# Optimization experiments

Hardware: AMD Instinct MI355X
Metric: run time of the kernel (lower is better)

## Reference

```python
import jax, jax.numpy as jnp
from jax import lax
import numpy as np

LEVEL_HW = [(100, 100), (50, 50), (25, 25), (13, 13), (7, 7)]  # P3..P7 for 800x800 input
N, C, A, K, NCONV = 2, 256, 9, 80, 4
PRIOR_PROB = 0.01


def conv3x3(x, w, b):
    # x: (N,C,H,W), w: (O,I,3,3), stride 1, pad 1
    y = lax.conv_general_dilated(x, w, (1, 1), 'SAME',
                                 dimension_numbers=('NCHW', 'OIHW', 'NCHW'))
    return y + b[None, :, None, None]


def permute_to_N_HWA_K(t, k):
    # (N, A*k, H, W) -> (N, H*W*A, k), matching the torch helper
    n, _, h, w = t.shape
    return t.reshape(n, -1, k, h, w).transpose(0, 3, 4, 1, 2).reshape(n, -1, k)


def setup_inputs() -> dict:
    key = jax.random.key(0)
    ks = iter(jax.random.split(key, 64))
    inp = {}
    for i, (h, w) in enumerate(LEVEL_HW):
        inp[f"f{i}"] = jax.random.normal(next(ks), (N, C, h, w), jnp.float32)
    for pre in ("cls", "box"):
        for i in range(NCONV):
            inp[f"{pre}_w{i}"] = 0.01 * jax.random.normal(next(ks), (C, C, 3, 3), jnp.float32)
            inp[f"{pre}_b{i}"] = jnp.zeros((C,), jnp.float32)
    bias_value = -float(np.log((1.0 - PRIOR_PROB) / PRIOR_PROB))
    inp["cls_score_w"] = 0.01 * jax.random.normal(next(ks), (A * K, C, 3, 3), jnp.float32)
    inp["cls_score_b"] = jnp.full((A * K,), bias_value, jnp.float32)
    inp["box_pred_w"] = 0.01 * jax.random.normal(next(ks), (A * 4, C, 3, 3), jnp.float32)
    inp["box_pred_b"] = jnp.zeros((A * 4,), jnp.float32)
    return inp


def reference(f0, f1, f2, f3, f4,
              cls_w0, cls_b0, cls_w1, cls_b1, cls_w2, cls_b2, cls_w3, cls_b3,
              box_w0, box_b0, box_w1, box_b1, box_w2, box_b2, box_w3, box_b3,
              cls_score_w, cls_score_b, box_pred_w, box_pred_b):
    feats = [f0, f1, f2, f3, f4]
    cls_p = [(cls_w0, cls_b0), (cls_w1, cls_b1), (cls_w2, cls_b2), (cls_w3, cls_b3)]
    box_p = [(box_w0, box_b0), (box_w1, box_b1), (box_w2, box_b2), (box_w3, box_b3)]
    logits, boxes = [], []
    for f in feats:
        x = f
        for w, b in cls_p:
            x = jax.nn.relu(conv3x3(x, w, b))
        logits.append(permute_to_N_HWA_K(conv3x3(x, cls_score_w, cls_score_b), K))
        y = f
        for w, b in box_p:
            y = jax.nn.relu(conv3x3(y, w, b))
        boxes.append(permute_to_N_HWA_K(conv3x3(y, box_pred_w, box_pred_b), 4))
    # (N, R, K) and (N, R, 4) with R = sum_l Hl*Wl*A = 120087; concat on last dim
    return jnp.concatenate([jnp.concatenate(logits, 1), jnp.concatenate(boxes, 1)], axis=2)
```

## Files before the change

kernel.cpp:

```cpp
#include <hip/hip_runtime.h>


typedef __attribute__((ext_vector_type(8))) short short8;
typedef __attribute__((ext_vector_type(4))) float floatx4;

#define LVLTOT 14143

__device__ __forceinline__ unsigned short f2bf(float f) {
  unsigned int u = __float_as_uint(f);
  unsigned int r = (u + 0x7fffu + ((u >> 16) & 1u)) >> 16;
  return (unsigned short)r;
}

__device__ __forceinline__ void gload_lds16(const void* g, void* l) {
  __builtin_amdgcn_global_load_lds(
      (const __attribute__((address_space(1))) unsigned int*)g,
      (__attribute__((address_space(3))) unsigned int*)l, 16, 0, 0);
}

__global__ __launch_bounds__(256) void xprep(
    const float* __restrict__ f, unsigned short* __restrict__ x0,
    int H, int W, int Wp, int lvloff) {
  __shared__ float ts[8][33];
  int t = threadIdx.x;
  int w0 = blockIdx.x * 32, h = blockIdx.y;
  int n = blockIdx.z >> 5, cbk = blockIdx.z & 31;
  int cl = t >> 5, wl = t & 31;
  float v = 0.f;
  if (w0 + wl < W)
    v = f[(((size_t)n * 256 + cbk * 8 + cl) * H + h) * W + w0 + wl];
  ts[cl][wl] = v;
  __syncthreads();
  int pi = t >> 3, cj = t & 7;
  if (w0 + pi < W)
    x0[((size_t)n * LVLTOT + lvloff + (size_t)(h + 1) * Wp + (w0 + pi + 1)) * 256 +
       cbk * 8 + cj] = f2bf(ts[cj][pi]);
}

struct WPArgs {
  const float* src[10];
  unsigned short* dst[10];
  int cout[10];
  int coutp[10];
};
__global__ __launch_bounds__(256) void wprep(WPArgs A) {
  int id = blockIdx.y;
  int idx = blockIdx.x * 256 + threadIdx.x;
  int coutp = A.coutp[id];
  if (idx >= coutp * 256) return;
  int co = idx >> 8, ci = idx & 255;
  const float* w = A.src[id];
  unsigned short* dst = A.dst[id];
  int cb = co >> 6, col = co & 63, chk = ci >> 5, qd = (ci >> 3) & 3, j = ci & 7;
  bool valid = co < A.cout[id];
#pragma unroll
  for (int tap = 0; tap < 9; tap++) {
    float v = valid ? w[((size_t)co * 256 + ci) * 9 + tap] : 0.f;
    dst[((((size_t)(cb * 8 + chk) * 9 + tap) * 4 + qd) * 64 + col) * 8 + j] = f2bf(v);
  }
}

__device__ __forceinline__ void decode_tile(int tile, int& l, int& h0, int& w0,
                                            int& H, int& W, int& Wp, int& loff) {
  const int Ht[5] = {100, 50, 25, 13, 7};
  const int Wpt[5] = {102, 52, 27, 15, 9};
  const int TXt[5] = {7, 4, 2, 1, 1};
  const int LOFFt[5] = {0, 10404, 13108, 13837, 14062};
  int tloc;
  if (tile < 49) { l = 0; tloc = tile; }
  else if (tile < 65) { l = 1; tloc = tile - 49; }
  else if (tile < 69) { l = 2; tloc = tile - 65; }
  else if (tile < 70) { l = 3; tloc = tile - 69; }
  else { l = 4; tloc = 0; }
  H = Ht[l]; W = H; Wp = Wpt[l]; loff = LOFFt[l];
  int ty = tloc / TXt[l], tx = tloc - ty * TXt[l];
  h0 = ty * 16; w0 = tx * 16;
}

#define CONV_MAIN_LOOP(INP, WBLOB, CB)                                          \
  for (int ch = 0; ch < 8; ch++) {                                              \
    if (ch) __syncthreads();                                                    \
    const unsigned short* wsrc = (WBLOB) + ((size_t)((CB)*8 + ch)) * 18432;     \
    _Pragma("unroll")                                                           \
    for (int i = 0; i < 9; i++)                                                 \
      gload_lds16(wsrc + i * 2048 + wv * 512 + lane * 8,                        \
                  lds_w + i * 2048 + wv * 512);                                 \
    _Pragma("unroll")                                                           \
    for (int g = 0; g < 6; g++) {                                               \
      int px = g * 64 + lane;                                                   \
      int r = px / 18, c = px - r * 18;                                         \
      int hh = h0 + r; if (hh > Hpad - 1) hh = Hpad - 1;                        \
      int ww = w0 + c; if (ww > Wp - 1) ww = Wp - 1;                            \
      gload_lds16((INP) + ((size_t)hh * Wp + ww) * 256 + ch * 32 + wv * 8,      \
                  lds_x + wv * 3072 + g * 512);                                 \
    }                                                                           \
    __syncthreads();                                                            \
    const short8* xw = (const short8*)lds_w;                                    \
    const short8* xx = (const short8*)lds_x;                                    \
    _Pragma("unroll")                                                           \
    for (int tap = 0; tap < 9; tap++) {                                         \
      const int tdy = tap / 3, tdx = tap - 3 * (tap / 3);                       \
      short8 bfr[4];                                                            \
      _Pragma("unroll")                                                         \
      for (int rr = 0; rr < 4; rr++)                                            \
        bfr[rr] = xx[q * 384 + (wv * 4 + rr + tdy) * 18 + n16 + tdx];           \
      _Pragma("unroll")                                                         \
      for (int cc = 0; cc < 4; cc++) {                                          \
        short8 afr = xw[(tap * 4 + q) * 64 + cc * 16 + n16];                    \
        _Pragma("unroll")                                                       \
        for (int rr = 0; rr < 4; rr++)                                          \
          acc[cc][rr] = __builtin_amdgcn_mfma_f32_16x16x32_bf16(                \
              afr, bfr[rr], acc[cc][rr], 0, 0, 0);                              \
      }                                                                         \
    }                                                                           \
  }

__global__ __launch_bounds__(256, 2) void conv_tower_mfma(
    const unsigned short* __restrict__ xin, unsigned short* __restrict__ xout,
    const unsigned short* __restrict__ wblob_cls,
    const unsigned short* __restrict__ wblob_box,
    const float* __restrict__ bias_cls, const float* __restrict__ bias_box,
    int in_n_stride, int in_tw_stride) {
  __shared__ __align__(16) unsigned short lds_w[18432];
  __shared__ __align__(16) unsigned short lds_x[12288];
  const int t = threadIdx.x, lane = t & 63, wv = t >> 6;
  const int q = lane >> 4, n16 = lane & 15;
  int l, h0, w0, H, W, Wp, loff;
  decode_tile(blockIdx.x, l, h0, w0, H, W, Wp, loff);
  const int Hpad = H + 2;
  const int cb = blockIdx.y;
  const int n = blockIdx.z >> 1, tw = blockIdx.z & 1;
  const unsigned short* wblob = tw ? wblob_box : wblob_cls;
  const float* bias = tw ? bias_box : bias_cls;
  const unsigned short* inp =
      xin + ((size_t)n * in_n_stride + (size_t)tw * in_tw_stride + loff) * 256;
  unsigned short* outp = xout + ((size_t)(n * 2 + tw) * LVLTOT + loff) * 256;

  floatx4 acc[4][4];
#pragma unroll
  for (int i = 0; i < 4; i++)
#pragma unroll
    for (int jj = 0; jj < 4; jj++) acc[i][jj] = (floatx4){0.f, 0.f, 0.f, 0.f};

  CONV_MAIN_LOOP(inp, wblob, cb)

#pragma unroll
  for (int cc = 0; cc < 4; cc++) {
    floatx4 bb = *(const floatx4*)(bias + cb * 64 + cc * 16 + q * 4);
#pragma unroll
    for (int rr = 0; rr < 4; rr++) {
      int h = h0 + wv * 4 + rr;
      int w_ = w0 + n16;
      if (h < H && w_ < W) {
        unsigned short pk[4];
#pragma unroll
        for (int rg = 0; rg < 4; rg++)
          pk[rg] = f2bf(fmaxf(acc[cc][rr][rg] + bb[rg], 0.f));
        size_t base =
            ((size_t)(h + 1) * Wp + (w_ + 1)) * 256 + cb * 64 + cc * 16 + q * 4;
        *(unsigned long long*)(outp + base) = *(unsigned long long*)pk;
      }
    }
  }
}

template <bool IS_CLS>
__global__ __launch_bounds__(256, 2) void conv_final_mfma(
    const unsigned short* __restrict__ xin, float* __restrict__ out,
    const unsigned short* __restrict__ wblob, const float* __restrict__ bias) {
  __shared__ __align__(16) unsigned short lds_w[18432];
  __shared__ __align__(16) unsigned short lds_x[12288];
  const int t = threadIdx.x, lane = t & 63, wv = t >> 6;
  const int q = lane >> 4, n16 = lane & 15;
  int l, h0, w0, H, W, Wp, loff;
  decode_tile(blockIdx.x, l, h0, w0, H, W, Wp, loff);
  const int Hpad = H + 2;
  const int cb = blockIdx.y;
  const int n = blockIdx.z;
  const int tw = IS_CLS ? 0 : 1;
  const int Cout = IS_CLS ? 720 : 36;
  const int RB[5] = {0, 90000, 112500, 118125, 119646};
  const unsigned short* inp = xin + ((size_t)(n * 2 + tw) * LVLTOT + loff) * 256;

  floatx4 acc[4][4];
#pragma unroll
  for (int i = 0; i < 4; i++)
#pragma unroll
    for (int jj = 0; jj < 4; jj++) acc[i][jj] = (floatx4){0.f, 0.f, 0.f, 0.f};

  CONV_MAIN_LOOP(inp, wblob, cb)

#pragma unroll
  for (int cc = 0; cc < 4; cc++) {
    int co0 = cb * 64 + cc * 16 + q * 4;
    if (co0 >= Cout) continue;
    floatx4 bb = *(const floatx4*)(bias + co0);
    int a = IS_CLS ? (co0 / 80) : (co0 >> 2);
    int col0 = IS_CLS ? (co0 - a * 80) : 80;
#pragma unroll
    for (int rr = 0; rr < 4; rr++) {
      int h = h0 + wv * 4 + rr;
      int w_ = w0 + n16;
      if (h < H && w_ < W) {
        size_t ridx = (size_t)RB[l] + ((size_t)h * W + w_) * 9 + a;
        floatx4 v;
#pragma unroll
        for (int rg = 0; rg < 4; rg++) v[rg] = acc[cc][rr][rg] + bb[rg];
        *(floatx4*)(out + ((size_t)n * 120087 + ridx) * 84 + col0) = v;
      }
    }
  }
}

extern "C" void kernel_launch(void* const* d_in, const int* in_sizes, int n_in,
                              void* d_out, int out_size, void* d_ws,
                              size_t ws_size, hipStream_t stream) {
  char* ws = (char*)d_ws;
  unsigned short* bufB = (unsigned short*)(ws);
  unsigned short* X0 = (unsigned short*)(ws + 14482432);
  unsigned short* bufA = (unsigned short*)(ws + 28964864);
  unsigned short* tb[8];
  for (int i = 0; i < 8; i++)
    tb[i] = (unsigned short*)(ws + 57929728 + (size_t)i * 1179648);
  unsigned short* fb_cls = (unsigned short*)(ws + 67366912);
  unsigned short* fb_box = (unsigned short*)(ws + 70905856);

  const float* f[5];
  for (int i = 0; i < 5; i++) f[i] = (const float*)d_in[i];
  float* out = (float*)d_out;

  hipMemsetAsync(ws, 0, 57929728, stream);

  const int Ht[5] = {100, 50, 25, 13, 7};
  const int Wpt[5] = {102, 52, 27, 15, 9};
  const int LOFFt[5] = {0, 10404, 13108, 13837, 14062};
  for (int l = 0; l < 5; l++) {
    dim3 g((Ht[l] + 31) / 32, Ht[l], 64);
    xprep<<<g, 256, 0, stream>>>(f[l], X0, Ht[l], Ht[l], Wpt[l], LOFFt[l]);
  }

  WPArgs wa;
  for (int i = 0; i < 4; i++) {
    wa.src[i] = (const float*)d_in[5 + 2 * i];
    wa.src[4 + i] = (const float*)d_in[13 + 2 * i];
    wa.dst[i] = tb[i];
    wa.dst[4 + i] = tb[4 + i];
    wa.cout[i] = wa.cout[4 + i] = 256;
    wa.coutp[i] = wa.coutp[4 + i] = 256;
  }
  wa.src[8] = (const float*)d_in[21]; wa.dst[8] = fb_cls;
  wa.cout[8] = 720; wa.coutp[8] = 768;
  wa.src[9] = (const float*)d_in[23]; wa.dst[9] = fb_box;
  wa.cout[9] = 36; wa.coutp[9] = 64;
  wprep<<<dim3(768, 10), 256, 0, stream>>>(wa);

  const float* cls_b[4], * box_b[4];
  for (int i = 0; i < 4; i++) {
    cls_b[i] = (const float*)d_in[6 + 2 * i];
    box_b[i] = (const float*)d_in[14 + 2 * i];
  }

  dim3 gt(71, 4, 4);
  conv_tower_mfma<<<gt, 256, 0, stream>>>(X0, bufA, tb[0], tb[4], cls_b[0],
                                          box_b[0], LVLTOT, 0);
  conv_tower_mfma<<<gt, 256, 0, stream>>>(bufA, bufB, tb[1], tb[5], cls_b[1],
                                          box_b[1], 2 * LVLTOT, LVLTOT);
  conv_tower_mfma<<<gt, 256, 0, stream>>>(bufB, bufA, tb[2], tb[6], cls_b[2],
                                          box_b[2], 2 * LVLTOT, LVLTOT);
  conv_tower_mfma<<<gt, 256, 0, stream>>>(bufA, bufB, tb[3], tb[7], cls_b[3],
                                          box_b[3], 2 * LVLTOT, LVLTOT);

  conv_final_mfma<true><<<dim3(71, 12, 2), 256, 0, stream>>>(
      bufB, out, fb_cls, (const float*)d_in[22]);
  conv_final_mfma<false><<<dim3(71, 1, 2), 256, 0, stream>>>(
      bufB, out, fb_box, (const float*)d_in[24]);
}
```

Measured before the change: 690.2 us.

## Switch conv MFMA to 32x32x16 tiles and zero only padding borders

Convolution kernels move from 16x16x32 to 32x32x16 bf16 MFMA, with a matching repacked weight layout and per-lane mapping; this cuts LDS fragment loads per MFMA. The full workspace memset is replaced by a kernel that zeroes only the padded border pixels of the activation planes. The five xprep launches are merged into one, the two final-head kernels are merged into one launch, and input offsets are hoisted out of the channel loop. The new lane mapping and weight layout must agree exactly, which is a correctness risk. Border zeroing relies on the activation planes being laid out contiguously.

```diff
diff --git a/kernel.cpp b/kernel.cpp
--- a/kernel.cpp
+++ b/kernel.cpp
@@ -3,6 +3,7 @@
 
 typedef __attribute__((ext_vector_type(8))) short short8;
 typedef __attribute__((ext_vector_type(4))) float floatx4;
+typedef __attribute__((ext_vector_type(16))) float floatx16;
 
 #define LVLTOT 14143
 
@@ -18,12 +19,47 @@
       (__attribute__((address_space(3))) unsigned int*)l, 16, 0, 0);
 }
 
+__global__ __launch_bounds__(256) void border_zero(
+    unsigned short* __restrict__ bufA, unsigned short* __restrict__ bufB) {
+  static const int Wpt[5] = {102, 52, 27, 15, 9};
+  static const int LOFFt[6] = {0, 10404, 13108, 13837, 14062, 14143};
+  int idx = blockIdx.x * 256 + threadIdx.x;
+  if (idx >= LVLTOT * 32) return;
+  int px = idx >> 5, oct = idx & 31;
+  int l = 0;
+  while (px >= LOFFt[l + 1]) l++;
+  int local = px - LOFFt[l];
+  int Wp = Wpt[l];
+  int r = local / Wp, c = local - r * Wp;
+  if (r != 0 && r != Wp - 1 && c != 0 && c != Wp - 1) return;
+  int plane = blockIdx.y;
+  unsigned short* base = (plane < 4)
+                             ? (bufA + (size_t)plane * LVLTOT * 256)
+                             : (bufB + (size_t)(plane - 4) * LVLTOT * 256);
+  floatx4 z;
+  z[0] = z[1] = z[2] = z[3] = 0.f;
+  *(floatx4*)(base + (size_t)px * 256 + oct * 8) = z;
+}
+
 __global__ __launch_bounds__(256) void xprep(
-    const float* __restrict__ f, unsigned short* __restrict__ x0,
-    int H, int W, int Wp, int lvloff) {
+    const float* __restrict__ f0, const float* __restrict__ f1,
+    const float* __restrict__ f2, const float* __restrict__ f3,
+    const float* __restrict__ f4, unsigned short* __restrict__ x0) {
+  static const int Ht[5] = {100, 50, 25, 13, 7};
+  static const int Wpt[5] = {102, 52, 27, 15, 9};
+  static const int LOFFt[5] = {0, 10404, 13108, 13837, 14062};
   __shared__ float ts[8][33];
+  int bx = blockIdx.x;
+  int l, h, wb;
+  if (bx < 400)      { l = 0; h = bx >> 2;         wb = bx & 3; }
+  else if (bx < 500) { l = 1; h = (bx - 400) >> 1; wb = (bx - 400) & 1; }
+  else if (bx < 525) { l = 2; h = bx - 500; wb = 0; }
+  else if (bx < 538) { l = 3; h = bx - 525; wb = 0; }
+  else               { l = 4; h = bx - 538; wb = 0; }
+  const float* f = l == 0 ? f0 : l == 1 ? f1 : l == 2 ? f2 : l == 3 ? f3 : f4;
+  int H = Ht[l], W = H, Wp = Wpt[l], loff = LOFFt[l];
   int t = threadIdx.x;
-  int w0 = blockIdx.x * 32, h = blockIdx.y;
+  int w0 = wb * 32;
   int n = blockIdx.z >> 5, cbk = blockIdx.z & 31;
   int cl = t >> 5, wl = t & 31;
   float v = 0.f;
@@ -33,7 +69,7 @@
   __syncthreads();
   int pi = t >> 3, cj = t & 7;
   if (w0 + pi < W)
-    x0[((size_t)n * LVLTOT + lvloff + (size_t)(h + 1) * Wp + (w0 + pi + 1)) * 256 +
+    x0[((size_t)n * LVLTOT + loff + (size_t)(h + 1) * Wp + (w0 + pi + 1)) * 256 +
        cbk * 8 + cj] = f2bf(ts[cj][pi]);
 }
 
@@ -51,12 +87,15 @@
   int co = idx >> 8, ci = idx & 255;
   const float* w = A.src[id];
   unsigned short* dst = A.dst[id];
-  int cb = co >> 6, col = co & 63, chk = ci >> 5, qd = (ci >> 3) & 3, j = ci & 7;
   bool valid = co < A.cout[id];
+  int cb = co >> 6, cc = (co >> 5) & 1, co32 = co & 31;
+  int ch = ci >> 5, ci5 = ci & 31;
+  int kk = ci5 >> 4, kh = (ci5 >> 3) & 1, j = ci5 & 7;
 #pragma unroll
   for (int tap = 0; tap < 9; tap++) {
     float v = valid ? w[((size_t)co * 256 + ci) * 9 + tap] : 0.f;
-    dst[((((size_t)(cb * 8 + chk) * 9 + tap) * 4 + qd) * 64 + col) * 8 + j] = f2bf(v);
+    dst[((((size_t)(cb * 8 + ch) * 9 + tap) * 2 + kk) * 2 + cc) * 512 +
+        kh * 256 + co32 * 8 + j] = f2bf(v);
   }
 }
 
@@ -77,42 +116,43 @@
   h0 = ty * 16; w0 = tx * 16;
 }
 
-#define CONV_MAIN_LOOP(INP, WBLOB, CB)                                          \
-  for (int ch = 0; ch < 8; ch++) {                                              \
-    if (ch) __syncthreads();                                                    \
-    const unsigned short* wsrc = (WBLOB) + ((size_t)((CB)*8 + ch)) * 18432;     \
-    _Pragma("unroll")                                                           \
-    for (int i = 0; i < 9; i++)                                                 \
-      gload_lds16(wsrc + i * 2048 + wv * 512 + lane * 8,                        \
-                  lds_w + i * 2048 + wv * 512);                                 \
-    _Pragma("unroll")                                                           \
-    for (int g = 0; g < 6; g++) {                                               \
-      int px = g * 64 + lane;                                                   \
-      int r = px / 18, c = px - r * 18;                                         \
-      int hh = h0 + r; if (hh > Hpad - 1) hh = Hpad - 1;                        \
-      int ww = w0 + c; if (ww > Wp - 1) ww = Wp - 1;                            \
-      gload_lds16((INP) + ((size_t)hh * Wp + ww) * 256 + ch * 32 + wv * 8,      \
-                  lds_x + wv * 3072 + g * 512);                                 \
-    }                                                                           \
-    __syncthreads();                                                            \
-    const short8* xw = (const short8*)lds_w;                                    \
-    const short8* xx = (const short8*)lds_x;                                    \
-    _Pragma("unroll")                                                           \
-    for (int tap = 0; tap < 9; tap++) {                                         \
-      const int tdy = tap / 3, tdx = tap - 3 * (tap / 3);                       \
-      short8 bfr[4];                                                            \
-      _Pragma("unroll")                                                         \
-      for (int rr = 0; rr < 4; rr++)                                            \
-        bfr[rr] = xx[q * 384 + (wv * 4 + rr + tdy) * 18 + n16 + tdx];           \
-      _Pragma("unroll")                                                         \
-      for (int cc = 0; cc < 4; cc++) {                                          \
-        short8 afr = xw[(tap * 4 + q) * 64 + cc * 16 + n16];                    \
-        _Pragma("unroll")                                                       \
-        for (int rr = 0; rr < 4; rr++)                                          \
-          acc[cc][rr] = __builtin_amdgcn_mfma_f32_16x16x32_bf16(                \
-              afr, bfr[rr], acc[cc][rr], 0, 0, 0);                              \
-      }                                                                         \
-    }                                                                           \
+#define CONV_MAIN_LOOP(INP, WBLOB, CB)                                         \
+  {                                                                            \
+    size_t xoff[6];                                                            \
+    _Pragma("unroll") for (int g = 0; g < 6; g++) {                            \
+      int px = g * 64 + lane;                                                  \
+      int r = px / 18, c = px - r * 18;                                        \
+      int hh = h0 + r; if (hh > Hpad - 1) hh = Hpad - 1;                       \
+      int ww = w0 + c; if (ww > Wp - 1) ww = Wp - 1;                           \
+      xoff[g] = ((size_t)hh * Wp + ww) * 256 + wv * 8;                         \
+    }                                                                          \
+    for (int ch = 0; ch < 8; ch++) {                                           \
+      if (ch) __syncthreads();                                                 \
+      const unsigned short* wsrc = (WBLOB) + ((size_t)((CB)*8 + ch)) * 18432;  \
+      _Pragma("unroll") for (int i = 0; i < 9; i++)                            \
+        gload_lds16(wsrc + i * 2048 + wv * 512 + lane * 8,                     \
+                    lds_w + i * 2048 + wv * 512);                              \
+      _Pragma("unroll") for (int g = 0; g < 6; g++)                            \
+        gload_lds16((INP) + xoff[g] + ch * 32, lds_x + wv * 3072 + g * 512);   \
+      __syncthreads();                                                         \
+      const short8* xw = (const short8*)lds_w;                                 \
+      const short8* xx = (const short8*)lds_x;                                 \
+      _Pragma("unroll") for (int tap = 0; tap < 9; tap++) {                    \
+        const int tdy = tap / 3, tdx = tap - 3 * (tap / 3);                    \
+        short8 bfr[2][2];                                                      \
+        _Pragma("unroll") for (int kk = 0; kk < 2; kk++)                       \
+          _Pragma("unroll") for (int rr = 0; rr < 2; rr++)                     \
+            bfr[kk][rr] = xx[(kk * 2 + kh) * 384 +                             \
+                             (wv * 4 + rr * 2 + rh + tdy) * 18 + n15 + tdx];   \
+        _Pragma("unroll") for (int kk = 0; kk < 2; kk++)                       \
+          _Pragma("unroll") for (int cc = 0; cc < 2; cc++) {                   \
+            short8 afr = xw[((tap * 2 + kk) * 2 + cc) * 64 + lane];            \
+            _Pragma("unroll") for (int rr = 0; rr < 2; rr++)                   \
+              acc[cc][rr] = __builtin_amdgcn_mfma_f32_32x32x16_bf16(           \
+                  afr, bfr[kk][rr], acc[cc][rr], 0, 0, 0);                     \
+          }                                                                    \
+      }                                                                        \
+    }                                                                          \
   }
 
 __global__ __launch_bounds__(256, 2) void conv_tower_mfma(
@@ -124,7 +164,7 @@
   __shared__ __align__(16) unsigned short lds_w[18432];
   __shared__ __align__(16) unsigned short lds_x[12288];
   const int t = threadIdx.x, lane = t & 63, wv = t >> 6;
-  const int q = lane >> 4, n16 = lane & 15;
+  const int kh = lane >> 5, rh = (lane >> 4) & 1, n15 = lane & 15;
   int l, h0, w0, H, W, Wp, loff;
   decode_tile(blockIdx.x, l, h0, w0, H, W, Wp, loff);
   const int Hpad = H + 2;
@@ -136,80 +176,93 @@
       xin + ((size_t)n * in_n_stride + (size_t)tw * in_tw_stride + loff) * 256;
   unsigned short* outp = xout + ((size_t)(n * 2 + tw) * LVLTOT + loff) * 256;
 
-  floatx4 acc[4][4];
-#pragma unroll
-  for (int i = 0; i < 4; i++)
-#pragma unroll
-    for (int jj = 0; jj < 4; jj++) acc[i][jj] = (floatx4){0.f, 0.f, 0.f, 0.f};
+  floatx16 acc[2][2];
+#pragma unroll
+  for (int i = 0; i < 2; i++)
+#pragma unroll
+    for (int jj = 0; jj < 2; jj++)
+#pragma unroll
+      for (int e = 0; e < 16; e++) acc[i][jj][e] = 0.f;
 
   CONV_MAIN_LOOP(inp, wblob, cb)
 
 #pragma unroll
-  for (int cc = 0; cc < 4; cc++) {
-    floatx4 bb = *(const floatx4*)(bias + cb * 64 + cc * 16 + q * 4);
-#pragma unroll
-    for (int rr = 0; rr < 4; rr++) {
-      int h = h0 + wv * 4 + rr;
-      int w_ = w0 + n16;
-      if (h < H && w_ < W) {
-        unsigned short pk[4];
-#pragma unroll
-        for (int rg = 0; rg < 4; rg++)
-          pk[rg] = f2bf(fmaxf(acc[cc][rr][rg] + bb[rg], 0.f));
-        size_t base =
-            ((size_t)(h + 1) * Wp + (w_ + 1)) * 256 + cb * 64 + cc * 16 + q * 4;
-        *(unsigned long long*)(outp + base) = *(unsigned long long*)pk;
+  for (int cc = 0; cc < 2; cc++)
+#pragma unroll
+    for (int r2 = 0; r2 < 4; r2++) {
+      int cob = cb * 64 + cc * 32 + 8 * r2 + 4 * kh;
+      floatx4 bb = *(const floatx4*)(bias + cob);
+#pragma unroll
+      for (int rr = 0; rr < 2; rr++) {
+        int h = h0 + wv * 4 + rr * 2 + rh;
+        int w_ = w0 + n15;
+        if (h < H && w_ < W) {
+          unsigned short pk[4];
+#pragma unroll
+          for (int q4 = 0; q4 < 4; q4++)
+            pk[q4] = f2bf(fmaxf(acc[cc][rr][r2 * 4 + q4] + bb[q4], 0.f));
+          *(unsigned long long*)(outp + ((size_t)(h + 1) * Wp + (w_ + 1)) * 256 +
+                                 cob) = *(unsigned long long*)pk;
+        }
       }
     }
-  }
-}
-
-template <bool IS_CLS>
+}
+
 __global__ __launch_bounds__(256, 2) void conv_final_mfma(
     const unsigned short* __restrict__ xin, float* __restrict__ out,
-    const unsigned short* __restrict__ wblob, const float* __restrict__ bias) {
+    const unsigned short* __restrict__ wblob_cls,
+    const unsigned short* __restrict__ wblob_box,
+    const float* __restrict__ bias_cls, const float* __restrict__ bias_box) {
   __shared__ __align__(16) unsigned short lds_w[18432];
   __shared__ __align__(16) unsigned short lds_x[12288];
   const int t = threadIdx.x, lane = t & 63, wv = t >> 6;
-  const int q = lane >> 4, n16 = lane & 15;
+  const int kh = lane >> 5, rh = (lane >> 4) & 1, n15 = lane & 15;
   int l, h0, w0, H, W, Wp, loff;
   decode_tile(blockIdx.x, l, h0, w0, H, W, Wp, loff);
   const int Hpad = H + 2;
-  const int cb = blockIdx.y;
+  const int yb = blockIdx.y;
+  const bool is_cls = yb < 12;
+  const int cb = is_cls ? yb : 0;
+  const int tw = is_cls ? 0 : 1;
+  const int Cout = is_cls ? 720 : 36;
+  const unsigned short* wblob = is_cls ? wblob_cls : wblob_box;
+  const float* bias = is_cls ? bias_cls : bias_box;
   const int n = blockIdx.z;
-  const int tw = IS_CLS ? 0 : 1;
-  const int Cout = IS_CLS ? 720 : 36;
   const int RB[5] = {0, 90000, 112500, 118125, 119646};
   const unsigned short* inp = xin + ((size_t)(n * 2 + tw) * LVLTOT + loff) * 256;
 
-  floatx4 acc[4][4];
-#pragma unroll
-  for (int i = 0; i < 4; i++)
-#pragma unroll
-    for (int jj = 0; jj < 4; jj++) acc[i][jj] = (floatx4){0.f, 0.f, 0.f, 0.f};
+  floatx16 acc[2][2];
+#pragma unroll
+  for (int i = 0; i < 2; i++)
+#pragma unroll
+    for (int jj = 0; jj < 2; jj++)
+#pragma unroll
+      for (int e = 0; e < 16; e++) acc[i][jj][e] = 0.f;
 
   CONV_MAIN_LOOP(inp, wblob, cb)
 
 #pragma unroll
-  for (int cc = 0; cc < 4; cc++) {
-    int co0 = cb * 64 + cc * 16 + q * 4;
-    if (co0 >= Cout) continue;
-    floatx4 bb = *(const floatx4*)(bias + co0);
-    int a = IS_CLS ? (co0 / 80) : (co0 >> 2);
-    int col0 = IS_CLS ? (co0 - a * 80) : 80;
-#pragma unroll
-    for (int rr = 0; rr < 4; rr++) {
-      int h = h0 + wv * 4 + rr;
-      int w_ = w0 + n16;
-      if (h < H && w_ < W) {
-        size_t ridx = (size_t)RB[l] + ((size_t)h * W + w_) * 9 + a;
-        floatx4 v;
-#pragma unroll
-        for (int rg = 0; rg < 4; rg++) v[rg] = acc[cc][rr][rg] + bb[rg];
-        *(floatx4*)(out + ((size_t)n * 120087 + ridx) * 84 + col0) = v;
+  for (int cc = 0; cc < 2; cc++)
+#pragma unroll
+    for (int r2 = 0; r2 < 4; r2++) {
+      int co0 = cb * 64 + cc * 32 + 8 * r2 + 4 * kh;
+      if (co0 >= Cout) continue;
+      floatx4 bb = *(const floatx4*)(bias + co0);
+      int a = is_cls ? (co0 / 80) : (co0 >> 2);
+      int col0 = is_cls ? (co0 - a * 80) : 80;
+#pragma unroll
+      for (int rr = 0; rr < 2; rr++) {
+        int h = h0 + wv * 4 + rr * 2 + rh;
+        int w_ = w0 + n15;
+        if (h < H && w_ < W) {
+          size_t ridx = (size_t)RB[l] + ((size_t)h * W + w_) * 9 + a;
+          floatx4 v;
+#pragma unroll
+          for (int q4 = 0; q4 < 4; q4++) v[q4] = acc[cc][rr][r2 * 4 + q4] + bb[q4];
+          *(floatx4*)(out + ((size_t)n * 120087 + ridx) * 84 + col0) = v;
+        }
       }
     }
-  }
 }
 
 extern "C" void kernel_launch(void* const* d_in, const int* in_sizes, int n_in,
@@ -225,19 +278,12 @@
   unsigned short* fb_cls = (unsigned short*)(ws + 67366912);
   unsigned short* fb_box = (unsigned short*)(ws + 70905856);
 
-  const float* f[5];
-  for (int i = 0; i < 5; i++) f[i] = (const float*)d_in[i];
   float* out = (float*)d_out;
 
-  hipMemsetAsync(ws, 0, 57929728, stream);
-
-  const int Ht[5] = {100, 50, 25, 13, 7};
-  const int Wpt[5] = {102, 52, 27, 15, 9};
-  const int LOFFt[5] = {0, 10404, 13108, 13837, 14062};
-  for (int l = 0; l < 5; l++) {
-    dim3 g((Ht[l] + 31) / 32, Ht[l], 64);
-    xprep<<<g, 256, 0, stream>>>(f[l], X0, Ht[l], Ht[l], Wpt[l], LOFFt[l]);
-  }
+  border_zero<<<dim3((LVLTOT * 32 + 255) / 256, 8), 256, 0, stream>>>(bufA, bufB);
+  xprep<<<dim3(545, 1, 64), 256, 0, stream>>>(
+      (const float*)d_in[0], (const float*)d_in[1], (const float*)d_in[2],
+      (const float*)d_in[3], (const float*)d_in[4], X0);
 
   WPArgs wa;
   for (int i = 0; i < 4; i++) {
@@ -254,7 +300,7 @@
   wa.cout[9] = 36; wa.coutp[9] = 64;
   wprep<<<dim3(768, 10), 256, 0, stream>>>(wa);
 
-  const float* cls_b[4], * box_b[4];
+  const float *cls_b[4], *box_b[4];
   for (int i = 0; i < 4; i++) {
     cls_b[i] = (const float*)d_in[6 + 2 * i];
     box_b[i] = (const float*)d_in[14 + 2 * i];
@@ -270,8 +316,6 @@
   conv_tower_mfma<<<gt, 256, 0, stream>>>(bufA, bufB, tb[3], tb[7], cls_b[3],
                                           box_b[3], 2 * LVLTOT, LVLTOT);
 
-  conv_final_mfma<true><<<dim3(71, 12, 2), 256, 0, stream>>>(
-      bufB, out, fb_cls, (const float*)d_in[22]);
-  conv_final_mfma<false><<<dim3(71, 1, 2), 256, 0, stream>>>(
-      bufB, out, fb_box, (const float*)d_in[24]);
-}
+  conv_final_mfma<<<dim3(71, 13, 2), 256, 0, stream>>>(
+      bufB, out, fb_cls, fb_box, (const float*)d_in[22], (const float*)d_in[24]);
+}
```

Result: slower. 707.4 us (+2.5%).
